# Performance work log

Hardware: AMD Instinct MI355X
Metric: run time of the kernel (lower is better)

Reference implementation:

```python
import jax, jax.numpy as jnp
import numpy as np

D_MODEL = 1024
N_HEADS = 16
D_HEAD = 64
SCALE = D_HEAD ** -0.5


def setup_inputs() -> dict:
    key = jax.random.key(0)
    k1, k2, k3, k4, k5 = jax.random.split(key, 5)
    B, N = 8, 1024
    x = jax.random.normal(k1, (B, N, D_MODEL), dtype=jnp.float32)
    qkv_w = jax.random.normal(k2, (3 * D_MODEL, D_MODEL), dtype=jnp.float32) * (D_MODEL ** -0.5)
    qkv_b = jax.random.normal(k3, (3 * D_MODEL,), dtype=jnp.float32) * 0.02
    proj_w = jax.random.normal(k4, (D_MODEL, D_MODEL), dtype=jnp.float32) * (D_MODEL ** -0.5)
    proj_b = jax.random.normal(k5, (D_MODEL,), dtype=jnp.float32) * 0.02
    return {"x": x, "qkv_w": qkv_w, "qkv_b": qkv_b, "proj_w": proj_w, "proj_b": proj_b}


def reference(x, qkv_w, qkv_b, proj_w, proj_b):
    B, N, C = x.shape
    # qkv projection (torch Linear: x @ W.T + b)
    qkv = x @ qkv_w.T + qkv_b                      # [B, N, 3*C]
    qkv = qkv.reshape(B, N, 3, N_HEADS, D_HEAD)
    qkv = jnp.transpose(qkv, (2, 0, 3, 1, 4))      # [3, B, H, N, d]
    q, k, v = qkv[0], qkv[1], qkv[2]
    q = q * SCALE
    attn_scores = jnp.einsum('bhqd,bhkd->bhqk', q, k)   # [B, H, N, N]
    attn_pattern = jax.nn.softmax(attn_scores, axis=-1)
    attn_pattern = jnp.where(jnp.isnan(attn_pattern), jnp.zeros_like(attn_pattern), attn_pattern)
    z = jnp.einsum('bhqk,bhkd->bhqd', attn_pattern, v)   # [B, H, N, d]
    z = jnp.transpose(z, (0, 2, 1, 3)).reshape(B, N, C)
    return z @ proj_w.T + proj_b
```

## Files before the change

kernel.cpp:

```cpp
#include <hip/hip_runtime.h>
#include <hip/hip_fp16.h>

typedef _Float16 half8 __attribute__((ext_vector_type(8)));
typedef _Float16 half4v __attribute__((ext_vector_type(4)));
typedef float f32x4 __attribute__((ext_vector_type(4)));

#define GAS1(p) ((const __attribute__((address_space(1))) void*)(p))
#define LAS3(p) ((__attribute__((address_space(3))) void*)(p))

#define SCALE 0.125f
#define LOG2E 1.44269504088896340736f
#define RESCALE_THR 8.0f

__global__ void cvt_f32_f16(const float* __restrict__ in, _Float16* __restrict__ out) {
  int i = blockIdx.x * 256 + threadIdx.x;
  float4 f = reinterpret_cast<const float4*>(in)[i];
  half4v h;
  h[0] = (_Float16)f.x; h[1] = (_Float16)f.y;
  h[2] = (_Float16)f.z; h[3] = (_Float16)f.w;
  reinterpret_cast<half4v*>(out)[i] = h;
}

template<int EPI>
__launch_bounds__(256, 2)
__global__ void gemm128(const _Float16* __restrict__ A, const _Float16* __restrict__ Bw,
                        const float* __restrict__ bias,
                        float* __restrict__ Cf,
                        _Float16* __restrict__ qo, _Float16* __restrict__ ko,
                        _Float16* __restrict__ vto,
                        int Kdim, int Ndim) {
  __shared__ alignas(128) _Float16 As[128 * 64];
  __shared__ alignas(128) _Float16 Bs[128 * 64];
  const int tid = threadIdx.x;
  const int w = tid >> 6, lane = tid & 63, lo = lane & 15, hi = lane >> 4;
  const int wr = w >> 1, wc = w & 1;
  const int tm0 = blockIdx.x * 128;
  const int tn0 = blockIdx.y * 128;

  f32x4 acc[4][4] = {};

  for (int k0 = 0; k0 < Kdim; k0 += 64) {
    __syncthreads();
#pragma unroll
    for (int r = 0; r < 4; ++r) {
      int o = r * 4096 + w * 1024 + lane * 16;
      int row = o >> 7;
      int kk = ((o & 127) ^ ((row & 7) << 4)) >> 1;
      __builtin_amdgcn_global_load_lds(GAS1(A + (size_t)(tm0 + row) * Kdim + k0 + kk),
                                       LAS3((char*)As + r * 4096 + w * 1024), 16, 0, 0);
      __builtin_amdgcn_global_load_lds(GAS1(Bw + (size_t)(tn0 + row) * Kdim + k0 + kk),
                                       LAS3((char*)Bs + r * 4096 + w * 1024), 16, 0, 0);
    }
    __syncthreads();
#pragma unroll
    for (int s = 0; s < 2; ++s) {
      half8 af[4], bf[4];
#pragma unroll
      for (int i = 0; i < 4; ++i) {
        int arow = wr * 64 + i * 16 + lo;
        int abyte = (arow << 7) + ((hi * 16 + s * 64) ^ ((arow & 7) << 4));
        af[i] = *reinterpret_cast<const half8*>((const char*)As + abyte);
        int brow = wc * 64 + i * 16 + lo;
        int bbyte = (brow << 7) + ((hi * 16 + s * 64) ^ ((brow & 7) << 4));
        bf[i] = *reinterpret_cast<const half8*>((const char*)Bs + bbyte);
      }
#pragma unroll
      for (int i = 0; i < 4; ++i)
#pragma unroll
        for (int j = 0; j < 4; ++j)
          acc[i][j] = __builtin_amdgcn_mfma_f32_16x16x32_f16(af[i], bf[j], acc[i][j], 0, 0, 0);
    }
  }

  if (EPI == 0) {
#pragma unroll
    for (int i = 0; i < 4; ++i) {
      const int m0 = tm0 + wr * 64 + i * 16 + hi * 4;
#pragma unroll
      for (int j = 0; j < 4; ++j) {
        const int n = tn0 + wc * 64 + j * 16 + lo;
        const float bj = bias[n];
#pragma unroll
        for (int r = 0; r < 4; ++r)
          Cf[(size_t)(m0 + r) * Ndim + n] = acc[i][j][r] + bj;
      }
    }
  } else {
    const int t = tn0 >> 10;
#pragma unroll
    for (int i = 0; i < 4; ++i) {
      const int m0 = tm0 + wr * 64 + i * 16 + hi * 4;
      const int b = m0 >> 10;
      const int nr = m0 & 1023;
#pragma unroll
      for (int j = 0; j < 4; ++j) {
        const int n = tn0 + wc * 64 + j * 16 + lo;
        const float bj = bias[n];
        const int h = (n >> 6) & 15;
        const int d = n & 63;
        const size_t hb = ((size_t)(b * 16 + h)) << 16;
        if (t == 0) {
#pragma unroll
          for (int r = 0; r < 4; ++r)
            qo[hb + (size_t)(nr + r) * 64 + d] = (_Float16)((acc[i][j][r] + bj) * SCALE);
        } else if (t == 1) {
#pragma unroll
          for (int r = 0; r < 4; ++r)
            ko[hb + (size_t)(nr + r) * 64 + d] = (_Float16)(acc[i][j][r] + bj);
        } else {
          half4v v4;
#pragma unroll
          for (int r = 0; r < 4; ++r) v4[r] = (_Float16)(acc[i][j][r] + bj);
          *reinterpret_cast<half4v*>(vto + hb + (size_t)d * 1024 + nr) = v4;
        }
      }
    }
  }
}

__launch_bounds__(256, 4)
__global__ void attn_kernel(const _Float16* __restrict__ q, const _Float16* __restrict__ kb,
                            const _Float16* __restrict__ vt, _Float16* __restrict__ z) {
  __shared__ alignas(128) _Float16 Ks[2][64 * 64];
  __shared__ alignas(128) _Float16 Vs[2][64 * 64];
  __shared__ alignas(128) _Float16 P[4][16 * 64];
  const int tid = threadIdx.x;
  const int w = tid >> 6, lane = tid & 63, lo = lane & 15, hi = lane >> 4;
  const int bh = blockIdx.y;
  const int qr0 = blockIdx.x * 128 + w * 32;
  const size_t base = (size_t)bh << 16;

  auto stage = [&](int buf, int kt) {
#pragma unroll
    for (int p = 0; p < 2; ++p) {
      int o = p * 4096 + w * 1024 + lane * 16;
      int row = o >> 7;
      int kk = ((o & 127) ^ ((row & 7) << 4)) >> 1;
      __builtin_amdgcn_global_load_lds(GAS1(kb + base + (size_t)(kt + row) * 64 + kk),
                                       LAS3((char*)&Ks[buf][0] + p * 4096 + w * 1024), 16, 0, 0);
      __builtin_amdgcn_global_load_lds(GAS1(vt + base + (size_t)row * 1024 + kt + kk),
                                       LAS3((char*)&Vs[buf][0] + p * 4096 + w * 1024), 16, 0, 0);
    }
  };

  stage(0, 0);

  half8 qf[2][2];
#pragma unroll
  for (int rg = 0; rg < 2; ++rg)
#pragma unroll
    for (int s = 0; s < 2; ++s)
      qf[rg][s] = *reinterpret_cast<const half8*>(
          q + base + (size_t)(qr0 + rg * 16 + lo) * 64 + s * 32 + hi * 8);

  f32x4 zacc[2][4] = {};
  float m_s[2] = {-1e30f, -1e30f};
  float l_s[2] = {0.f, 0.f};

  char* Pw = (char*)&P[w][0];
  __syncthreads();

  int buf = 0;
  for (int kt = 0; kt < 1024; kt += 64) {
    if (kt + 64 < 1024) stage(buf ^ 1, kt + 64);
    const char* Kb = (const char*)&Ks[buf][0];
    const char* Vb = (const char*)&Vs[buf][0];

    f32x4 sacc[2][4];
#pragma unroll
    for (int rg = 0; rg < 2; ++rg)
#pragma unroll
      for (int c = 0; c < 4; ++c) sacc[rg][c] = f32x4{0.f, 0.f, 0.f, 0.f};
#pragma unroll
    for (int c = 0; c < 4; ++c) {
      const int row = c * 16 + lo;
      half8 bK0 = *reinterpret_cast<const half8*>(
          Kb + (row << 7) + ((hi * 16) ^ ((row & 7) << 4)));
      half8 bK1 = *reinterpret_cast<const half8*>(
          Kb + (row << 7) + ((64 + hi * 16) ^ ((row & 7) << 4)));
      __builtin_amdgcn_s_setprio(1);
#pragma unroll
      for (int rg = 0; rg < 2; ++rg) {
        sacc[rg][c] = __builtin_amdgcn_mfma_f32_16x16x32_f16(bK0, qf[rg][0], sacc[rg][c], 0, 0, 0);
        sacc[rg][c] = __builtin_amdgcn_mfma_f32_16x16x32_f16(bK1, qf[rg][1], sacc[rg][c], 0, 0, 0);
      }
      __builtin_amdgcn_s_setprio(0);
    }

#pragma unroll
    for (int rg = 0; rg < 2; ++rg) {
      float tmax = fmaxf(
          fmaxf(fmaxf(fmaxf(sacc[rg][0][0], sacc[rg][0][1]), fmaxf(sacc[rg][0][2], sacc[rg][0][3])),
                fmaxf(fmaxf(sacc[rg][1][0], sacc[rg][1][1]), fmaxf(sacc[rg][1][2], sacc[rg][1][3]))),
          fmaxf(fmaxf(fmaxf(sacc[rg][2][0], sacc[rg][2][1]), fmaxf(sacc[rg][2][2], sacc[rg][2][3])),
                fmaxf(fmaxf(sacc[rg][3][0], sacc[rg][3][1]), fmaxf(sacc[rg][3][2], sacc[rg][3][3]))));
      if (!__all(tmax <= m_s[rg] + RESCALE_THR)) {
        float t2 = fmaxf(tmax, __shfl_xor(tmax, 16));
        t2 = fmaxf(t2, __shfl_xor(t2, 32));
        float mn = fmaxf(m_s[rg], t2);
        float alpha = exp2f((m_s[rg] - mn) * LOG2E);
        m_s[rg] = mn;
        l_s[rg] *= alpha;
#pragma unroll
        for (int v = 0; v < 4; ++v)
#pragma unroll
          for (int u = 0; u < 4; ++u) zacc[rg][v][u] *= alpha;
      }
      const float ml = m_s[rg] * LOG2E;
      float psum = 0.f;
#pragma unroll
      for (int c = 0; c < 4; ++c)
#pragma unroll
        for (int u = 0; u < 4; ++u) {
          float p = exp2f(sacc[rg][c][u] * LOG2E - ml);
          sacc[rg][c][u] = p;
          psum += p;
        }
      l_s[rg] += psum;

#pragma unroll
      for (int c = 0; c < 4; ++c) {
        half4v p4;
#pragma unroll
        for (int u = 0; u < 4; ++u) p4[u] = (_Float16)sacc[rg][c][u];
        int byteoff = (lo << 7) + ((c * 32 + hi * 8) ^ ((lo & 7) << 4));
        *reinterpret_cast<half4v*>(Pw + byteoff) = p4;
      }

#pragma unroll
      for (int s = 0; s < 2; ++s) {
        int pbyte = (lo << 7) + ((hi * 16 + s * 64) ^ ((lo & 7) << 4));
        half8 pf = *reinterpret_cast<const half8*>((const char*)Pw + pbyte);
        half8 bV[4];
#pragma unroll
        for (int v = 0; v < 4; ++v) {
          int row = v * 16 + lo;
          bV[v] = *reinterpret_cast<const half8*>(
              Vb + (row << 7) + ((s * 64 + hi * 16) ^ ((row & 7) << 4)));
        }
        __builtin_amdgcn_s_setprio(1);
#pragma unroll
        for (int v = 0; v < 4; ++v)
          zacc[rg][v] = __builtin_amdgcn_mfma_f32_16x16x32_f16(bV[v], pf, zacc[rg][v], 0, 0, 0);
        __builtin_amdgcn_s_setprio(0);
      }
    }
    __syncthreads();
    buf ^= 1;
  }

  const int b = bh >> 4, h = bh & 15;
#pragma unroll
  for (int rg = 0; rg < 2; ++rg) {
    float l = l_s[rg];
    l += __shfl_xor(l, 16);
    l += __shfl_xor(l, 32);
    const float rl = 1.0f / l;
    const int qrow = qr0 + rg * 16 + lo;
#pragma unroll
    for (int v = 0; v < 4; ++v) {
      half4v o;
#pragma unroll
      for (int u = 0; u < 4; ++u) o[u] = (_Float16)(zacc[rg][v][u] * rl);
      *reinterpret_cast<half4v*>(
          z + ((size_t)b * 1024 + qrow) * 1024 + h * 64 + v * 16 + hi * 4) = o;
    }
  }
}

extern "C" void kernel_launch(void* const* d_in, const int* in_sizes, int n_in,
                              void* d_out, int out_size, void* d_ws, size_t ws_size,
                              hipStream_t stream) {
  const float* x      = (const float*)d_in[0];
  const float* qkv_w  = (const float*)d_in[1];
  const float* qkv_b  = (const float*)d_in[2];
  const float* proj_w = (const float*)d_in[3];
  const float* proj_b = (const float*)d_in[4];
  float* out = (float*)d_out;

  _Float16* ws    = (_Float16*)d_ws;
  _Float16* xb    = ws;
  _Float16* wqkv  = ws + 8388608;
  _Float16* wproj = ws + 11534336;
  _Float16* qb    = ws + 12582912;
  _Float16* kbb   = ws + 20971520;
  _Float16* vtb   = ws + 29360128;
  _Float16* zb    = ws + 37748736;

  cvt_f32_f16<<<8192, 256, 0, stream>>>(x, xb);
  cvt_f32_f16<<<3072, 256, 0, stream>>>(qkv_w, wqkv);
  cvt_f32_f16<<<1024, 256, 0, stream>>>(proj_w, wproj);

  gemm128<1><<<dim3(64, 24), 256, 0, stream>>>(xb, wqkv, qkv_b, nullptr,
                                               qb, kbb, vtb, 1024, 3072);
  attn_kernel<<<dim3(8, 128), 256, 0, stream>>>(qb, kbb, vtb, zb);
  gemm128<0><<<dim3(64, 8), 256, 0, stream>>>(zb, wproj, proj_b, out,
                                              nullptr, nullptr, nullptr, 1024, 1024);
}
```

Baseline: 245.5 us.

## Replace 128x128 GEMM with pipelined 256x256 eight-wave GEMM and merge conversions

Replaces the 128x128, 4-wave GEMM with a 256x256, 8-wave GEMM. It double-buffers its LDS tiles and prefetches the next K tiles with async global-to-LDS loads while MFMAs run. Split barriers, partial waitcnts and setprio are used to interleave loads and compute. The three fp32-to-fp16 conversion launches are merged into one kernel to cut launch overhead. The larger tiles reduce global reloads per FLOP, but the projection GEMM now launches only 128 blocks, which may leave many CUs idle. The QKV GEMM's 384 blocks give an uneven tail.

Result: slower. 262.2 us (+6.8%).

```diff
diff --git a/kernel.cpp b/kernel.cpp
--- a/kernel.cpp
+++ b/kernel.cpp
@@ -12,105 +12,187 @@
 #define LOG2E 1.44269504088896340736f
 #define RESCALE_THR 8.0f
 
-__global__ void cvt_f32_f16(const float* __restrict__ in, _Float16* __restrict__ out) {
-  int i = blockIdx.x * 256 + threadIdx.x;
-  float4 f = reinterpret_cast<const float4*>(in)[i];
+__global__ void cvt_all(const float* __restrict__ x, const float* __restrict__ qw,
+                        const float* __restrict__ pw, _Float16* __restrict__ xb,
+                        _Float16* __restrict__ wqkv, _Float16* __restrict__ wproj) {
+  const int b = blockIdx.x;
+  const float* src;
+  _Float16* dst;
+  int j;
+  if (b < 8192)       { src = x;  dst = xb;    j = b * 256 + threadIdx.x; }
+  else if (b < 11264) { src = qw; dst = wqkv;  j = (b - 8192) * 256 + threadIdx.x; }
+  else                { src = pw; dst = wproj; j = (b - 11264) * 256 + threadIdx.x; }
+  float4 f = reinterpret_cast<const float4*>(src)[j];
   half4v h;
   h[0] = (_Float16)f.x; h[1] = (_Float16)f.y;
   h[2] = (_Float16)f.z; h[3] = (_Float16)f.w;
-  reinterpret_cast<half4v*>(out)[i] = h;
+  reinterpret_cast<half4v*>(dst)[j] = h;
 }
 
 template<int EPI>
-__launch_bounds__(256, 2)
-__global__ void gemm128(const _Float16* __restrict__ A, const _Float16* __restrict__ Bw,
-                        const float* __restrict__ bias,
-                        float* __restrict__ Cf,
+__launch_bounds__(512, 1)
+__global__ void gemm256(const _Float16* __restrict__ A, const _Float16* __restrict__ Bw,
+                        const float* __restrict__ bias, float* __restrict__ Cf,
                         _Float16* __restrict__ qo, _Float16* __restrict__ ko,
-                        _Float16* __restrict__ vto,
-                        int Kdim, int Ndim) {
-  __shared__ alignas(128) _Float16 As[128 * 64];
-  __shared__ alignas(128) _Float16 Bs[128 * 64];
+                        _Float16* __restrict__ vto, int Kdim, int Ndim) {
+  __shared__ alignas(128) _Float16 lds[2][2][2][128 * 64];
   const int tid = threadIdx.x;
   const int w = tid >> 6, lane = tid & 63, lo = lane & 15, hi = lane >> 4;
-  const int wr = w >> 1, wc = w & 1;
-  const int tm0 = blockIdx.x * 128;
-  const int tn0 = blockIdx.y * 128;
-
-  f32x4 acc[4][4] = {};
-
-  for (int k0 = 0; k0 < Kdim; k0 += 64) {
-    __syncthreads();
-#pragma unroll
-    for (int r = 0; r < 4; ++r) {
-      int o = r * 4096 + w * 1024 + lane * 16;
+  const int wm = w >> 2, wn = w & 3;
+  const int tm0 = blockIdx.x * 256, tn0 = blockIdx.y * 256;
+  const int T = Kdim >> 6;
+
+  auto stage = [&](int op, int t, int half) {
+    const _Float16* src = (op ? Bw + (size_t)(tn0 + half * 128) * Kdim
+                              : A + (size_t)(tm0 + half * 128) * Kdim) + t * 64;
+    char* dst = (char*)&lds[t & 1][op][half][0] + w * 1024;
+#pragma unroll
+    for (int qq = 0; qq < 2; ++qq) {
+      int o = qq * 8192 + w * 1024 + lane * 16;
       int row = o >> 7;
       int kk = ((o & 127) ^ ((row & 7) << 4)) >> 1;
-      __builtin_amdgcn_global_load_lds(GAS1(A + (size_t)(tm0 + row) * Kdim + k0 + kk),
-                                       LAS3((char*)As + r * 4096 + w * 1024), 16, 0, 0);
-      __builtin_amdgcn_global_load_lds(GAS1(Bw + (size_t)(tn0 + row) * Kdim + k0 + kk),
-                                       LAS3((char*)Bs + r * 4096 + w * 1024), 16, 0, 0);
-    }
-    __syncthreads();
-#pragma unroll
-    for (int s = 0; s < 2; ++s) {
-      half8 af[4], bf[4];
-#pragma unroll
-      for (int i = 0; i < 4; ++i) {
-        int arow = wr * 64 + i * 16 + lo;
-        int abyte = (arow << 7) + ((hi * 16 + s * 64) ^ ((arow & 7) << 4));
-        af[i] = *reinterpret_cast<const half8*>((const char*)As + abyte);
-        int brow = wc * 64 + i * 16 + lo;
-        int bbyte = (brow << 7) + ((hi * 16 + s * 64) ^ ((brow & 7) << 4));
-        bf[i] = *reinterpret_cast<const half8*>((const char*)Bs + bbyte);
-      }
-#pragma unroll
-      for (int i = 0; i < 4; ++i)
-#pragma unroll
-        for (int j = 0; j < 4; ++j)
-          acc[i][j] = __builtin_amdgcn_mfma_f32_16x16x32_f16(af[i], bf[j], acc[i][j], 0, 0, 0);
+      __builtin_amdgcn_global_load_lds(GAS1(src + (size_t)row * Kdim + kk),
+                                       LAS3(dst + qq * 8192), 16, 0, 0);
+    }
+  };
+
+  f32x4 acc[8][4] = {};
+
+  stage(0, 0, 0); stage(0, 0, 1); stage(1, 0, 0); stage(1, 0, 1);
+  stage(1, 1, 0); stage(1, 1, 1);
+  asm volatile("s_waitcnt vmcnt(0)" ::: "memory");
+  __builtin_amdgcn_sched_barrier(0);
+  __builtin_amdgcn_s_barrier();
+  __builtin_amdgcn_sched_barrier(0);
+
+  for (int t = 0; t < T; ++t) {
+    const char* Ab = (const char*)&lds[t & 1][0][wm][0];
+    const char* Bb = (const char*)&lds[t & 1][1][wn >> 1][0];
+    const int nrow0 = (wn & 1) * 64;
+    half8 af[4][2], bf[4][2];
+
+#pragma unroll
+    for (int m = 0; m < 4; ++m) {
+      int row = m * 16 + lo;
+#pragma unroll
+      for (int s = 0; s < 2; ++s)
+        af[m][s] = *reinterpret_cast<const half8*>(
+            Ab + (row << 7) + ((s * 64 + hi * 16) ^ ((row & 7) << 4)));
+    }
+#pragma unroll
+    for (int n = 0; n < 2; ++n) {
+      int row = nrow0 + n * 16 + lo;
+#pragma unroll
+      for (int s = 0; s < 2; ++s)
+        bf[n][s] = *reinterpret_cast<const half8*>(
+            Bb + (row << 7) + ((s * 64 + hi * 16) ^ ((row & 7) << 4)));
+    }
+    if (t + 1 < T) stage(0, t + 1, 0);
+    __builtin_amdgcn_sched_barrier(0);
+    __builtin_amdgcn_s_barrier();
+    __builtin_amdgcn_sched_barrier(0);
+    __builtin_amdgcn_s_setprio(1);
+#pragma unroll
+    for (int m = 0; m < 4; ++m)
+#pragma unroll
+      for (int n = 0; n < 2; ++n)
+#pragma unroll
+        for (int s = 0; s < 2; ++s)
+          acc[m][n] = __builtin_amdgcn_mfma_f32_16x16x32_f16(af[m][s], bf[n][s], acc[m][n], 0, 0, 0);
+    __builtin_amdgcn_s_setprio(0);
+
+#pragma unroll
+    for (int n = 2; n < 4; ++n) {
+      int row = nrow0 + n * 16 + lo;
+#pragma unroll
+      for (int s = 0; s < 2; ++s)
+        bf[n][s] = *reinterpret_cast<const half8*>(
+            Bb + (row << 7) + ((s * 64 + hi * 16) ^ ((row & 7) << 4)));
+    }
+    if (t + 1 < T) stage(0, t + 1, 1);
+    __builtin_amdgcn_sched_barrier(0);
+    __builtin_amdgcn_s_barrier();
+    __builtin_amdgcn_sched_barrier(0);
+    __builtin_amdgcn_s_setprio(1);
+#pragma unroll
+    for (int m = 0; m < 4; ++m)
+#pragma unroll
+      for (int n = 2; n < 4; ++n)
+#pragma unroll
+        for (int s = 0; s < 2; ++s)
+          acc[m][n] = __builtin_amdgcn_mfma_f32_16x16x32_f16(af[m][s], bf[n][s], acc[m][n], 0, 0, 0);
+    __builtin_amdgcn_s_setprio(0);
+
+#pragma unroll
+    for (int m = 0; m < 4; ++m) {
+      int row = 64 + m * 16 + lo;
+#pragma unroll
+      for (int s = 0; s < 2; ++s)
+        af[m][s] = *reinterpret_cast<const half8*>(
+            Ab + (row << 7) + ((s * 64 + hi * 16) ^ ((row & 7) << 4)));
+    }
+    if (t + 2 < T) { stage(1, t + 2, 0); stage(1, t + 2, 1); }
+    __builtin_amdgcn_sched_barrier(0);
+    __builtin_amdgcn_s_barrier();
+    __builtin_amdgcn_sched_barrier(0);
+    __builtin_amdgcn_s_setprio(1);
+#pragma unroll
+    for (int m = 0; m < 4; ++m)
+#pragma unroll
+      for (int n = 0; n < 4; ++n)
+#pragma unroll
+        for (int s = 0; s < 2; ++s)
+          acc[4 + m][n] = __builtin_amdgcn_mfma_f32_16x16x32_f16(af[m][s], bf[n][s], acc[4 + m][n], 0, 0, 0);
+    __builtin_amdgcn_s_setprio(0);
+
+    if (t + 1 < T) {
+      if (t + 2 < T) asm volatile("s_waitcnt vmcnt(4)" ::: "memory");
+      else           asm volatile("s_waitcnt vmcnt(0)" ::: "memory");
+      __builtin_amdgcn_sched_barrier(0);
+      __builtin_amdgcn_s_barrier();
+      __builtin_amdgcn_sched_barrier(0);
     }
   }
 
   if (EPI == 0) {
 #pragma unroll
-    for (int i = 0; i < 4; ++i) {
-      const int m0 = tm0 + wr * 64 + i * 16 + hi * 4;
-#pragma unroll
-      for (int j = 0; j < 4; ++j) {
-        const int n = tn0 + wc * 64 + j * 16 + lo;
-        const float bj = bias[n];
-#pragma unroll
-        for (int r = 0; r < 4; ++r)
-          Cf[(size_t)(m0 + r) * Ndim + n] = acc[i][j][r] + bj;
+    for (int M = 0; M < 8; ++M) {
+      const int gm = tm0 + wm * 128 + M * 16 + hi * 4;
+#pragma unroll
+      for (int n = 0; n < 4; ++n) {
+        const int gc = tn0 + wn * 64 + n * 16 + lo;
+        const float bj = bias[gc];
+#pragma unroll
+        for (int u = 0; u < 4; ++u)
+          Cf[(size_t)(gm + u) * Ndim + gc] = acc[M][n][u] + bj;
       }
     }
   } else {
-    const int t = tn0 >> 10;
-#pragma unroll
-    for (int i = 0; i < 4; ++i) {
-      const int m0 = tm0 + wr * 64 + i * 16 + hi * 4;
-      const int b = m0 >> 10;
-      const int nr = m0 & 1023;
-#pragma unroll
-      for (int j = 0; j < 4; ++j) {
-        const int n = tn0 + wc * 64 + j * 16 + lo;
-        const float bj = bias[n];
-        const int h = (n >> 6) & 15;
-        const int d = n & 63;
+    const int tsel = tn0 >> 10;
+#pragma unroll
+    for (int M = 0; M < 8; ++M) {
+      const int gm = tm0 + wm * 128 + M * 16 + hi * 4;
+      const int b = gm >> 10;
+      const int nr = gm & 1023;
+#pragma unroll
+      for (int n = 0; n < 4; ++n) {
+        const int gc = tn0 + wn * 64 + n * 16 + lo;
+        const float bj = bias[gc];
+        const int h = (gc >> 6) & 15;
+        const int d = gc & 63;
         const size_t hb = ((size_t)(b * 16 + h)) << 16;
-        if (t == 0) {
-#pragma unroll
-          for (int r = 0; r < 4; ++r)
-            qo[hb + (size_t)(nr + r) * 64 + d] = (_Float16)((acc[i][j][r] + bj) * SCALE);
-        } else if (t == 1) {
-#pragma unroll
-          for (int r = 0; r < 4; ++r)
-            ko[hb + (size_t)(nr + r) * 64 + d] = (_Float16)(acc[i][j][r] + bj);
+        if (tsel == 0) {
+#pragma unroll
+          for (int u = 0; u < 4; ++u)
+            qo[hb + (size_t)(nr + u) * 64 + d] = (_Float16)((acc[M][n][u] + bj) * SCALE);
+        } else if (tsel == 1) {
+#pragma unroll
+          for (int u = 0; u < 4; ++u)
+            ko[hb + (size_t)(nr + u) * 64 + d] = (_Float16)(acc[M][n][u] + bj);
         } else {
           half4v v4;
 #pragma unroll
-          for (int r = 0; r < 4; ++r) v4[r] = (_Float16)(acc[i][j][r] + bj);
+          for (int u = 0; u < 4; ++u) v4[u] = (_Float16)(acc[M][n][u] + bj);
           *reinterpret_cast<half4v*>(vto + hb + (size_t)d * 1024 + nr) = v4;
         }
       }
@@ -287,13 +369,11 @@
   _Float16* vtb   = ws + 29360128;
   _Float16* zb    = ws + 37748736;
 
-  cvt_f32_f16<<<8192, 256, 0, stream>>>(x, xb);
-  cvt_f32_f16<<<3072, 256, 0, stream>>>(qkv_w, wqkv);
-  cvt_f32_f16<<<1024, 256, 0, stream>>>(proj_w, wproj);
-
-  gemm128<1><<<dim3(64, 24), 256, 0, stream>>>(xb, wqkv, qkv_b, nullptr,
+  cvt_all<<<12288, 256, 0, stream>>>(x, qkv_w, proj_w, xb, wqkv, wproj);
+
+  gemm256<1><<<dim3(32, 12), 512, 0, stream>>>(xb, wqkv, qkv_b, nullptr,
                                                qb, kbb, vtb, 1024, 3072);
   attn_kernel<<<dim3(8, 128), 256, 0, stream>>>(qb, kbb, vtb, zb);
-  gemm128<0><<<dim3(64, 8), 256, 0, stream>>>(zb, wproj, proj_b, out,
+  gemm256<0><<<dim3(32, 4), 512, 0, stream>>>(zb, wproj, proj_b, out,
                                               nullptr, nullptr, nullptr, 1024, 1024);
 }
```
